# Kernel tuning notes

Measured on AMD Instinct MI355X. Metric: run time of the kernel, lower is better.

Reference implementation:

```python
import jax, jax.numpy as jnp
import numpy as np

B, S, D = 4096, 200, 64
H1, H2 = 80, 40


def setup_inputs() -> dict:
    key = jax.random.key(0)
    ks = jax.random.split(key, 9)
    seq = jax.random.normal(ks[0], (B, S, D), dtype=jnp.float32)
    tgt = jax.random.normal(ks[1], (B, D), dtype=jnp.float32)
    mask = jax.random.randint(ks[2], (B, S), 0, 2, dtype=jnp.int32)
    # MLP params: (4*D -> H1 -> H2 -> 1), glorot-ish init
    def lin(k, fan_in, fan_out):
        s = (2.0 / (fan_in + fan_out)) ** 0.5
        return jax.random.normal(k, (fan_in, fan_out), dtype=jnp.float32) * s
    W1 = lin(ks[3], 4 * D, H1)
    b1 = jnp.zeros((H1,), dtype=jnp.float32)
    W2 = lin(ks[4], H1, H2)
    b2 = jnp.zeros((H2,), dtype=jnp.float32)
    W3 = lin(ks[5], H2, 1)
    b3 = jnp.zeros((1,), dtype=jnp.float32)
    return {"sequence_emb": seq, "target_emb": tgt, "mask": mask,
            "W1": W1, "b1": b1, "W2": W2, "b2": b2, "W3": W3, "b3": b3}


def reference(sequence_emb, target_emb, mask, W1, b1, W2, b2, W3, b3):
    # DIN attention: concat[target, seq, target-seq, target*seq] -> MLP -> mask -> softmax
    t = target_emb[:, None, :]                                   # [B,1,D] broadcast over S
    t_full = jnp.broadcast_to(t, sequence_emb.shape)             # [B,S,D]
    din = jnp.concatenate(
        [t_full, sequence_emb, t_full - sequence_emb, t_full * sequence_emb],
        axis=-1)                                                 # [B,S,4D]
    h = jax.nn.relu(jnp.einsum('bsi,ij->bsj', din, W1) + b1)     # [B,S,H1]
    h = jax.nn.relu(jnp.einsum('bsi,ij->bsj', h, W2) + b2)       # [B,S,H2]
    score = (jnp.einsum('bsi,ij->bsj', h, W3) + b3)[..., 0]      # [B,S]
    m = mask.astype(score.dtype)
    score = score * m + (-1e9) * (1.0 - m)
    return jax.nn.softmax(score, axis=-1)
```

## Files before the change

### kernel.cpp

```cpp
#include <hip/hip_runtime.h>
#include <hip/hip_bf16.h>


#define WS_WCT   0
#define WS_W2T   20480
#define WS_B2P   29696
#define WS_W3P   29888
#define WS_U     30080

typedef __attribute__((ext_vector_type(8))) short short8;
typedef __attribute__((ext_vector_type(4))) float f32x4;

static __device__ __forceinline__ unsigned short f2bf(float f) {
    unsigned int u = __builtin_bit_cast(unsigned int, f);
    u = (u + 0x7FFFu + ((u >> 16) & 1u)) >> 16;
    return (unsigned short)u;
}

static __device__ __forceinline__ short8 pk8(float4 a, float4 b) {
    short8 r;
    r[0] = (short)f2bf(a.x); r[1] = (short)f2bf(a.y);
    r[2] = (short)f2bf(a.z); r[3] = (short)f2bf(a.w);
    r[4] = (short)f2bf(b.x); r[5] = (short)f2bf(b.y);
    r[6] = (short)f2bf(b.z); r[7] = (short)f2bf(b.w);
    return r;
}

__global__ __launch_bounds__(256) void prep_w_kernel(
    const float* __restrict__ W1, const float* __restrict__ W2,
    const float* __restrict__ b2, const float* __restrict__ W3,
    unsigned char* __restrict__ ws)
{
    const int tid = threadIdx.x;
    unsigned short* wcT = (unsigned short*)(ws + WS_WCT);
    for (int idx = tid; idx < 80 * 128; idx += 256) {
        int c = idx >> 7, k = idx & 127;
        float v;
        if (k < 64) v = W1[(64 + k) * 80 + c] - W1[(128 + k) * 80 + c];
        else        v = W1[(192 + (k - 64)) * 80 + c];
        wcT[(c << 7) + (k ^ ((c & 7) << 3))] = f2bf(v);
    }
    unsigned short* w2T = (unsigned short*)(ws + WS_W2T);
    for (int idx = tid; idx < 48 * 96; idx += 256) {
        int c2 = idx / 96, ks = idx - c2 * 96;
        int kt = ks >> 5, kq = (ks >> 3) & 3, e = ks & 7;
        int chan = 32 * kt + 16 * (e >> 2) + 4 * kq + (e & 3);
        float v = (c2 < 40 && chan < 80) ? W2[chan * 40 + c2] : 0.0f;
        w2T[idx] = f2bf(v);
    }
    float* b2p = (float*)(ws + WS_B2P);
    float* w3p = (float*)(ws + WS_W3P);
    for (int idx = tid; idx < 48; idx += 256) {
        b2p[idx] = (idx < 40) ? b2[idx] : 0.0f;
        w3p[idx] = (idx < 40) ? W3[idx] : 0.0f;
    }
    float* Uf = (float*)(ws + WS_U);
    for (int idx = tid; idx < 64 * 80; idx += 256) {
        int d = idx / 80, h = idx - d * 80;
        Uf[idx] = W1[d * 80 + h] + W1[(128 + d) * 80 + h];
    }
}

__global__ __launch_bounds__(256, 2) void score_kernel(
    const float* __restrict__ seq, const float* __restrict__ tgt,
    const float* __restrict__ b1g, const unsigned char* __restrict__ ws,
    float* __restrict__ out)
{
    __shared__ __align__(16) unsigned char w1s[20480];

    const int tid = threadIdx.x;
    {
        const float4* s1 = (const float4*)(ws + WS_WCT);
        float4* d1 = (float4*)w1s;
        #pragma unroll
        for (int i = 0; i < 5; ++i) d1[tid + 256 * i] = s1[tid + 256 * i];
    }

    const int l  = tid & 63;
    const int w  = tid >> 6;
    const int cb = l & 15;
    const int kq = l >> 4;
    const int swi = (cb & 7) << 4;

    const unsigned short* w2T = (const unsigned short*)(ws + WS_W2T);
    short8 bL2[3][3];
    #pragma unroll
    for (int kt = 0; kt < 3; ++kt)
        #pragma unroll
        for (int mt = 0; mt < 3; ++mt)
            bL2[kt][mt] = *(const short8*)(w2T + (cb + 16 * mt) * 96 + kt * 32 + kq * 8);
    const float* b2p = (const float*)(ws + WS_B2P);
    const float* w3p = (const float*)(ws + WS_W3P);
    float bw[3][4], wv[3][4];
    #pragma unroll
    for (int mt = 0; mt < 3; ++mt)
        #pragma unroll
        for (int j = 0; j < 4; ++j) {
            int c2 = mt * 16 + kq * 4 + j;
            bw[mt][j] = b2p[c2]; wv[mt][j] = w3p[c2];
        }
    __syncthreads();

    const int b = blockIdx.x * 4 + w;

    const float* tp = tgt + (size_t)b * 64 + kq * 8;
    const float4 T0 = *(const float4*)tp;        const float4 T1 = *(const float4*)(tp + 4);
    const float4 T2 = *(const float4*)(tp + 32); const float4 T3 = *(const float4*)(tp + 36);

    float biasOld[5];
    #pragma unroll
    for (int nt = 0; nt < 5; ++nt) biasOld[nt] = b1g[nt * 16 + cb];
    {
        const float* Uf = (const float*)(ws + WS_U);
        const float* tb = tgt + (size_t)b * 64;
        #pragma unroll 4
        for (int d = 0; d < 64; ++d) {
            float tA = tb[d];
            #pragma unroll
            for (int nt = 0; nt < 5; ++nt)
                biasOld[nt] += tA * Uf[d * 80 + nt * 16 + cb];
        }
    }
    float biasN[5][4];
    #pragma unroll
    for (int nt = 0; nt < 5; ++nt)
        #pragma unroll
        for (int j = 0; j < 4; ++j)
            biasN[nt][j] = __shfl(biasOld[nt], ((l >> 4) << 2) + j, 64);

#define STAGE(TT, S0,S1,S2,S3) do {                                            \
        int row = (TT) * 16 + cb; row = row > 199 ? 199 : row;                 \
        const float* sp = seq + ((size_t)b * 200 + row) * 64 + kq * 8;         \
        S0 = *(const float4*)sp;        S1 = *(const float4*)(sp + 4);         \
        S2 = *(const float4*)(sp + 32); S3 = *(const float4*)(sp + 36);        \
    } while (0)

#define PROC(TT, S0,S1,S2,S3) do {                                            \
        short8 a0 = pk8(S0, S1), a1 = pk8(S2, S3);                             \
        short8 a2 = pk8(T0 * S0, T1 * S1), a3 = pk8(T2 * S2, T3 * S3);         \
        f32x4 acc[5];                                                          \
        _Pragma("unroll")                                                      \
        for (int nt = 0; nt < 5; ++nt) {                                       \
            acc[nt][0] = biasN[nt][0]; acc[nt][1] = biasN[nt][1];              \
            acc[nt][2] = biasN[nt][2]; acc[nt][3] = biasN[nt][3];              \
        }                                                                      \
        _Pragma("unroll")                                                      \
        for (int kt = 0; kt < 4; ++kt) {                                       \
            short8 av = kt == 0 ? a0 : kt == 1 ? a1 : kt == 2 ? a2 : a3;       \
            _Pragma("unroll")                                                  \
            for (int nt = 0; nt < 5; ++nt) {                                   \
                short8 bf = *(const short8*)(w1s + (cb + 16 * nt) * 256 +      \
                                             ((kt * 64 + kq * 16) ^ swi));     \
                acc[nt] = __builtin_amdgcn_mfma_f32_16x16x32_bf16(bf, av, acc[nt], 0, 0, 0); \
            }                                                                  \
        }                                                                      \
        uint2 p[5];                                                            \
        _Pragma("unroll")                                                      \
        for (int nt = 0; nt < 5; ++nt) {                                       \
            float h0 = fmaxf(acc[nt][0], 0.0f), h1 = fmaxf(acc[nt][1], 0.0f);  \
            float h2 = fmaxf(acc[nt][2], 0.0f), h3 = fmaxf(acc[nt][3], 0.0f);  \
            p[nt].x = (unsigned)f2bf(h0) | ((unsigned)f2bf(h1) << 16);         \
            p[nt].y = (unsigned)f2bf(h2) | ((unsigned)f2bf(h3) << 16);         \
        }                                                                      \
        f32x4 acc2[3];                                                         \
        _Pragma("unroll")                                                      \
        for (int mt = 0; mt < 3; ++mt) {                                       \
            acc2[mt][0] = bw[mt][0]; acc2[mt][1] = bw[mt][1];                  \
            acc2[mt][2] = bw[mt][2]; acc2[mt][3] = bw[mt][3];                  \
        }                                                                      \
        _Pragma("unroll")                                                      \
        for (int kt = 0; kt < 3; ++kt) {                                       \
            uint4 bb;                                                          \
            bb.x = p[2 * kt].x; bb.y = p[2 * kt].y;                            \
            bb.z = (kt < 2) ? p[2 * kt + 1].x : 0u;                            \
            bb.w = (kt < 2) ? p[2 * kt + 1].y : 0u;                            \
            short8 b2f = __builtin_bit_cast(short8, bb);                       \
            _Pragma("unroll")                                                  \
            for (int mt = 0; mt < 3; ++mt)                                     \
                acc2[mt] = __builtin_amdgcn_mfma_f32_16x16x32_bf16(bL2[kt][mt], b2f, acc2[mt], 0, 0, 0); \
        }                                                                      \
        float part = 0.0f;                                                     \
        _Pragma("unroll")                                                      \
        for (int mt = 0; mt < 3; ++mt)                                         \
            _Pragma("unroll")                                                  \
            for (int j = 0; j < 4; ++j)                                        \
                part += fmaxf(acc2[mt][j], 0.0f) * wv[mt][j];                  \
        part += __shfl_xor(part, 16, 64);                                      \
        part += __shfl_xor(part, 32, 64);                                      \
        if (l < 16) {                                                          \
            int row = (TT) * 16 + cb;                                          \
            if (row < 200) out[(size_t)b * 200 + row] = part;                  \
        }                                                                      \
    } while (0)

    float4 sa0, sa1, sa2, sa3;
    float4 sb0, sb1, sb2, sb3;
    STAGE(0, sa0, sa1, sa2, sa3);
    #pragma unroll 1
    for (int i = 0; i < 6; ++i) {
        STAGE(2 * i + 1, sb0, sb1, sb2, sb3);
        PROC(2 * i,     sa0, sa1, sa2, sa3);
        STAGE(2 * i + 2, sa0, sa1, sa2, sa3);
        PROC(2 * i + 1, sb0, sb1, sb2, sb3);
    }
    PROC(12, sa0, sa1, sa2, sa3);
}

__global__ __launch_bounds__(256) void softmax_kernel(
    const int* __restrict__ mask, float* __restrict__ out)
{
    const int l = threadIdx.x & 63;
    const int w = threadIdx.x >> 6;
    const int b = blockIdx.x * 4 + w;
    float* po = out + (size_t)b * 200;
    const int* pm = mask + (size_t)b * 200;
    float v[4];
    #pragma unroll
    for (int j = 0; j < 4; ++j) {
        int tk = l + 64 * j;
        v[j] = (tk < 200) ? (pm[tk] ? po[tk] : -1.0e9f) : -3.0e38f;
    }
    float mx = fmaxf(fmaxf(v[0], v[1]), fmaxf(v[2], v[3]));
    #pragma unroll
    for (int st = 32; st >= 1; st >>= 1) mx = fmaxf(mx, __shfl_xor(mx, st, 64));
    float e[4], sm = 0.0f;
    #pragma unroll
    for (int j = 0; j < 4; ++j) {
        int tk = l + 64 * j;
        e[j] = (tk < 200) ? __expf(v[j] - mx) : 0.0f;
        sm += e[j];
    }
    #pragma unroll
    for (int st = 32; st >= 1; st >>= 1) sm += __shfl_xor(sm, st, 64);
    float inv = 1.0f / sm;
    #pragma unroll
    for (int j = 0; j < 4; ++j) {
        int tk = l + 64 * j;
        if (tk < 200) po[tk] = e[j] * inv;
    }
}

extern "C" void kernel_launch(void* const* d_in, const int* in_sizes, int n_in,
                              void* d_out, int out_size, void* d_ws, size_t ws_size,
                              hipStream_t stream)
{
    const float* seq = (const float*)d_in[0];
    const float* tgt = (const float*)d_in[1];
    const int*   msk = (const int*)d_in[2];
    const float* W1  = (const float*)d_in[3];
    const float* b1  = (const float*)d_in[4];
    const float* W2  = (const float*)d_in[5];
    const float* b2  = (const float*)d_in[6];
    const float* W3  = (const float*)d_in[7];
    unsigned char* ws = (unsigned char*)d_ws;
    float* out = (float*)d_out;

    prep_w_kernel<<<1, 256, 0, stream>>>(W1, W2, b2, W3, ws);
    score_kernel<<<1024, 256, 0, stream>>>(seq, tgt, b1, ws, out);
    softmax_kernel<<<1024, 256, 0, stream>>>(msk, out);
}
```

Before: 89.48 us.

## Move W2/bias weights to LDS and deepen sequence prefetch to three tiles

Moves the layer-2 weights, layer-2 bias and W3 vector out of per-thread registers into padded shared memory, reading them inside each tile step. The freed registers fund a third prefetch buffer, so sequence tiles are loaded three steps ahead instead of one. The aim is to hide more of the global load latency on the seq stream. The cost is extra LDS reads on every tile, and the LDS footprint grows, which could limit occupancy.

```diff
diff --git a/kernel.cpp b/kernel.cpp
--- a/kernel.cpp
+++ b/kernel.cpp
@@ -67,6 +67,9 @@
     float* __restrict__ out)
 {
     __shared__ __align__(16) unsigned char w1s[20480];
+    __shared__ __align__(16) unsigned short w2s[48 * 104];
+    __shared__ __align__(16) float bwS[48];
+    __shared__ __align__(16) float wvS[48];
 
     const int tid = threadIdx.x;
     {
@@ -74,6 +77,16 @@
         float4* d1 = (float4*)w1s;
         #pragma unroll
         for (int i = 0; i < 5; ++i) d1[tid + 256 * i] = s1[tid + 256 * i];
+        const unsigned int* s2 = (const unsigned int*)(ws + WS_W2T);
+        unsigned int* d2 = (unsigned int*)w2s;
+        for (int idx = tid; idx < 2304; idx += 256) {
+            int c2 = idx / 48, kk = idx - 48 * c2;
+            d2[c2 * 52 + kk] = s2[idx];
+        }
+        if (tid < 48) {
+            bwS[tid] = ((const float*)(ws + WS_B2P))[tid];
+            wvS[tid] = ((const float*)(ws + WS_W3P))[tid];
+        }
     }
 
     const int l  = tid & 63;
@@ -81,27 +94,7 @@
     const int cb = l & 15;
     const int kq = l >> 4;
     const int swi = (cb & 7) << 4;
-
-    const unsigned short* w2T = (const unsigned short*)(ws + WS_W2T);
-    short8 bL2[3][3];
-    #pragma unroll
-    for (int kt = 0; kt < 3; ++kt)
-        #pragma unroll
-        for (int mt = 0; mt < 3; ++mt)
-            bL2[kt][mt] = *(const short8*)(w2T + (cb + 16 * mt) * 96 + kt * 32 + kq * 8);
-    const float* b2p = (const float*)(ws + WS_B2P);
-    const float* w3p = (const float*)(ws + WS_W3P);
-    float bw[3][4], wv[3][4];
-    #pragma unroll
-    for (int mt = 0; mt < 3; ++mt)
-        #pragma unroll
-        for (int j = 0; j < 4; ++j) {
-            int c2 = mt * 16 + kq * 4 + j;
-            bw[mt][j] = b2p[c2]; wv[mt][j] = w3p[c2];
-        }
-    __syncthreads();
-
-    const int b = blockIdx.x * 4 + w;
+    const int b  = blockIdx.x * 4 + w;
 
     const float* tp = tgt + (size_t)b * 64 + kq * 8;
     const float4 T0 = *(const float4*)tp;        const float4 T1 = *(const float4*)(tp + 4);
@@ -128,6 +121,8 @@
         for (int j = 0; j < 4; ++j)
             biasN[nt][j] = __shfl(biasOld[nt], ((l >> 4) << 2) + j, 64);
 
+    __syncthreads();
+
 #define STAGE(TT, S0,S1,S2,S3) do {                                            \
         int row = (TT) * 16 + cb; row = row > 199 ? 199 : row;                 \
         const float* sp = seq + ((size_t)b * 200 + row) * 64 + kq * 8;         \
@@ -135,9 +130,13 @@
         S2 = *(const float4*)(sp + 32); S3 = *(const float4*)(sp + 36);        \
     } while (0)
 
-#define PROC(TT, S0,S1,S2,S3) do {                                            \
+#define STEP(T, DOSTAGE, S0,S1,S2,S3) do {                                     \
         short8 a0 = pk8(S0, S1), a1 = pk8(S2, S3);                             \
         short8 a2 = pk8(T0 * S0, T1 * S1), a3 = pk8(T2 * S2, T3 * S3);         \
+        if (DOSTAGE) {                                                         \
+            int tn = (T) + 3; tn = tn > 12 ? 12 : tn;                          \
+            STAGE(tn, S0, S1, S2, S3);                                         \
+        }                                                                      \
         f32x4 acc[5];                                                          \
         _Pragma("unroll")                                                      \
         for (int nt = 0; nt < 5; ++nt) {                                       \
@@ -164,10 +163,8 @@
         }                                                                      \
         f32x4 acc2[3];                                                         \
         _Pragma("unroll")                                                      \
-        for (int mt = 0; mt < 3; ++mt) {                                       \
-            acc2[mt][0] = bw[mt][0]; acc2[mt][1] = bw[mt][1];                  \
-            acc2[mt][2] = bw[mt][2]; acc2[mt][3] = bw[mt][3];                  \
-        }                                                                      \
+        for (int mt = 0; mt < 3; ++mt)                                         \
+            acc2[mt] = *(const f32x4*)(bwS + mt * 16 + kq * 4);                \
         _Pragma("unroll")                                                      \
         for (int kt = 0; kt < 3; ++kt) {                                       \
             uint4 bb;                                                          \
@@ -176,34 +173,41 @@
             bb.w = (kt < 2) ? p[2 * kt + 1].y : 0u;                            \
             short8 b2f = __builtin_bit_cast(short8, bb);                       \
             _Pragma("unroll")                                                  \
-            for (int mt = 0; mt < 3; ++mt)                                     \
-                acc2[mt] = __builtin_amdgcn_mfma_f32_16x16x32_bf16(bL2[kt][mt], b2f, acc2[mt], 0, 0, 0); \
+            for (int mt = 0; mt < 3; ++mt) {                                   \
+                short8 w2f = *(const short8*)(w2s + (cb + 16 * mt) * 104 +     \
+                                              kt * 32 + kq * 8);               \
+                acc2[mt] = __builtin_amdgcn_mfma_f32_16x16x32_bf16(w2f, b2f, acc2[mt], 0, 0, 0); \
+            }                                                                  \
         }                                                                      \
         float part = 0.0f;                                                     \
         _Pragma("unroll")                                                      \
-        for (int mt = 0; mt < 3; ++mt)                                         \
+        for (int mt = 0; mt < 3; ++mt) {                                       \
+            f32x4 wvv = *(const f32x4*)(wvS + mt * 16 + kq * 4);               \
             _Pragma("unroll")                                                  \
             for (int j = 0; j < 4; ++j)                                        \
-                part += fmaxf(acc2[mt][j], 0.0f) * wv[mt][j];                  \
+                part += fmaxf(acc2[mt][j], 0.0f) * wvv[j];                     \
+        }                                                                      \
         part += __shfl_xor(part, 16, 64);                                      \
         part += __shfl_xor(part, 32, 64);                                      \
         if (l < 16) {                                                          \
-            int row = (TT) * 16 + cb;                                          \
+            int row = (T) * 16 + cb;                                           \
             if (row < 200) out[(size_t)b * 200 + row] = part;                  \
         }                                                                      \
     } while (0)
 
     float4 sa0, sa1, sa2, sa3;
     float4 sb0, sb1, sb2, sb3;
+    float4 sc0, sc1, sc2, sc3;
     STAGE(0, sa0, sa1, sa2, sa3);
+    STAGE(1, sb0, sb1, sb2, sb3);
+    STAGE(2, sc0, sc1, sc2, sc3);
     #pragma unroll 1
-    for (int i = 0; i < 6; ++i) {
-        STAGE(2 * i + 1, sb0, sb1, sb2, sb3);
-        PROC(2 * i,     sa0, sa1, sa2, sa3);
-        STAGE(2 * i + 2, sa0, sa1, sa2, sa3);
-        PROC(2 * i + 1, sb0, sb1, sb2, sb3);
-    }
-    PROC(12, sa0, sa1, sa2, sa3);
+    for (int g = 0; g < 4; ++g) {
+        STEP(3 * g,     1, sa0, sa1, sa2, sa3);
+        STEP(3 * g + 1, 1, sb0, sb1, sb2, sb3);
+        STEP(3 * g + 2, 1, sc0, sc1, sc2, sc3);
+    }
+    STEP(12, 0, sa0, sa1, sa2, sa3);
 }
 
 __global__ __launch_bounds__(256) void softmax_kernel(
```

Measured after the change: 132.6 us. +48.2%, slower.
